# Optimization experiments

Hardware: AMD Instinct MI355X
Metric: run time of the kernel (lower is better)

## Reference

```python
import jax, jax.numpy as jnp
import numpy as np

N_NODES = 50000
N_EDGES = 800000
MUL0, MUL1 = 16, 8            # multiplicities of 0e and 1o irreps (input == output)
DIM_F = MUL0 + 3 * MUL1       # 40
NRB, NRD = 16, 64             # num_radial_basis, num_radial_dimension
MAX_RADIUS = 5.0
W_NUMEL = MUL0*MUL0 + MUL0*MUL1 + MUL1*MUL1 + MUL1*MUL0  # 576


def _radial_embedding(r):
    # e3nn soft_one_hot_linspace(basis='smooth_finite', cutoff=True), then *sqrt(NRB)
    values = jnp.linspace(0.0, MAX_RADIUS, NRB + 2)[1:-1]
    step = MAX_RADIUS / (NRB + 1)
    d = (r[:, None] - values) / step            # [E, NRB]
    inside = jnp.abs(d) < 1.0
    ds = jnp.where(inside, d, 0.0)              # safe values for the division
    y = 1.14136 * jnp.exp(jnp.float32(2.0)) * jnp.exp(-1.0 / (1.0 + ds)) * jnp.exp(-1.0 / (1.0 - ds))
    return jnp.where(inside, y, 0.0) * jnp.sqrt(jnp.float32(NRB))


def _forward(pos, f_in, W1, W2, edge_src, edge_dst):
    E = edge_src.shape[0]
    N = pos.shape[0]
    # edge geometry
    vec = pos[edge_dst] - pos[edge_src]                       # [E,3]
    r = jnp.sqrt(jnp.sum(vec * vec, axis=1) + 1e-12)          # [E]
    unit = vec / r[:, None]
    sh1 = jnp.sqrt(jnp.float32(3.0)) * unit                   # l=1 SH, component norm; sh0 == 1
    # radial MLP -> per-edge tensor-product weights (e3nn FullyConnectedNet scaling)
    emb = _radial_embedding(r)                                # [E, NRB]
    h = jax.nn.silu(emb @ W1 / jnp.sqrt(jnp.float32(NRB)))    # [E, NRD]
    w = h @ W2 / jnp.sqrt(jnp.float32(NRD))                   # [E, W_NUMEL]
    # gather source node features
    x = f_in[edge_src]                                        # [E, DIM_F]
    x0 = x[:, :MUL0]                                          # [E, 16] scalars (0e)
    x1 = x[:, MUL0:].reshape(E, MUL1, 3)                      # [E, 8, 3] vectors (1o)
    # split per-path 'uvw' weights
    o = MUL0 * MUL0
    w_00 = w[:, :o].reshape(E, MUL0, MUL0)                    # 0e x 0e -> 0e
    w_01 = w[:, o:o + MUL0*MUL1].reshape(E, MUL0, MUL1); o += MUL0*MUL1  # 0e x 1o -> 1o
    w_10 = w[:, o:o + MUL1*MUL1].reshape(E, MUL1, MUL1); o += MUL1*MUL1  # 1o x 0e -> 1o
    w_11 = w[:, o:o + MUL1*MUL0].reshape(E, MUL1, MUL0)                  # 1o x 1o -> 0e
    # path normalization: alpha = sqrt((2*l_out+1)/fan_in); fan_in per output = MUL0 + MUL1
    inv_fan = 1.0 / jnp.sqrt(jnp.float32(MUL0 + MUL1))
    inv_s3 = 1.0 / jnp.sqrt(jnp.float32(3.0))
    # scalar (0e) outputs
    dot = jnp.einsum('euk,ek->eu', x1, sh1)                   # [E, MUL1]
    out0 = inv_fan * (jnp.einsum('euw,eu->ew', w_00, x0)
                      + inv_s3 * jnp.einsum('euw,eu->ew', w_11, dot))
    # vector (1o) outputs
    out1 = inv_fan * (jnp.einsum('euw,eu->ew', w_01, x0)[:, :, None] * sh1[:, None, :]
                      + jnp.einsum('euw,euk->ewk', w_10, x1))
    summand = jnp.concatenate([out0, out1.reshape(E, 3 * MUL1)], axis=1)  # [E, DIM_F]
    f_out = jax.ops.segment_sum(summand, edge_dst, num_segments=N)
    num_neighbors = E / N
    return f_out / jnp.sqrt(jnp.float32(num_neighbors))


def setup_inputs() -> dict:
    key = jax.random.key(0)
    k1, k2, k3, k4, k5, k6 = jax.random.split(key, 6)
    pos = jax.random.normal(k1, (N_NODES, 3), dtype=jnp.float32)
    f_in = jax.random.normal(k2, (N_NODES, DIM_F), dtype=jnp.float32)
    edge_src = jax.random.randint(k3, (N_EDGES,), 0, N_NODES, dtype=jnp.int32)
    edge_dst = jax.random.randint(k4, (N_EDGES,), 0, N_NODES, dtype=jnp.int32)
    W1 = jax.random.normal(k5, (NRB, NRD), dtype=jnp.float32)
    W2 = jax.random.normal(k6, (NRD, W_NUMEL), dtype=jnp.float32)
    return {"pos": pos, "f_in": f_in, "edge_src": edge_src, "edge_dst": edge_dst, "W1": W1, "W2": W2}


def reference(pos, f_in, edge_src, edge_dst, W1, W2):
    return _forward(pos, f_in, W1, W2, edge_src, edge_dst)
```

## Files before the change

### kernel.cpp

```cpp
#include <hip/hip_runtime.h>
#include <hip/hip_fp16.h>

#define N_NODES 50000
#define N_EDGES 800000

typedef short  bf16x8 __attribute__((ext_vector_type(8)));
typedef float  f32x4  __attribute__((ext_vector_type(4)));
typedef _Float16 h16x2 __attribute__((ext_vector_type(2)));

#define FXP32_SCALE 4194304.0f
#define FXP32_INV   2.384185791015625e-07f

#define WSB_BYTES   (36864 * 2)

__device__ __forceinline__ unsigned short f2bf(float f) {
    unsigned u = __float_as_uint(f);
    u += 0x7FFF + ((u >> 16) & 1);
    return (unsigned short)(u >> 16);
}

__device__ __forceinline__ f32x4 fma4(f32x4 a, f32x4 b, f32x4 c) {
    f32x4 r;
    r[0] = fmaf(a[0], b[0], c[0]);
    r[1] = fmaf(a[1], b[1], c[1]);
    r[2] = fmaf(a[2], b[2], c[2]);
    r[3] = fmaf(a[3], b[3], c[3]);
    return r;
}

#if __has_builtin(__builtin_amdgcn_fdot2)
__device__ __forceinline__ float FDOT2(h16x2 a, h16x2 b, float c) {
    return __builtin_amdgcn_fdot2(a, b, c, false);
}
#else
__device__ __forceinline__ float FDOT2(h16x2 a, h16x2 b, float c) {
    return fmaf((float)a.x, (float)b.x, fmaf((float)a.y, (float)b.y, c));
}
#endif

__global__ void setup_kernel(const float* __restrict__ W2,
                             const float* __restrict__ W1,
                             unsigned short* __restrict__ wsB,
                             unsigned* __restrict__ w1p,
                             int4* __restrict__ out, int n16) {
    int gid = blockIdx.x * 256 + threadIdx.x;
    for (int i = gid; i < n16; i += gridDim.x * 256)
        out[i] = make_int4(0, 0, 0, 0);
    if (gid < 36864) {
        int j    = gid & 7;
        int lane = (gid >> 3) & 63;
        int ks   = (gid >> 9) & 1;
        int nt   = gid >> 10;
        int k = ks * 32 + (lane >> 4) * 8 + j;
        int n = nt * 16 + (lane & 15);
        wsB[gid] = f2bf(W2[k * 576 + n]);
    } else if (gid < 36864 + 512) {
        int idx = gid - 36864;
        int kk  = idx >> 6;
        int i   = idx & 63;
        __half lo = __float2half(W1[(2*kk)     * 64 + i]);
        __half hi = __float2half(W1[(2*kk + 1) * 64 + i]);
        w1p[idx] = (unsigned)__half_as_ushort(lo)
                 | ((unsigned)__half_as_ushort(hi) << 16);
    }
}

__global__ void finalize_kernel(float4* p, int n4) {
    int i = blockIdx.x * blockDim.x + threadIdx.x;
    if (i < n4) {
        float4 v = p[i];
        float4 f;
        f.x = (float)__float_as_int(v.x) * FXP32_INV;
        f.y = (float)__float_as_int(v.y) * FXP32_INV;
        f.z = (float)__float_as_int(v.z) * FXP32_INV;
        f.w = (float)__float_as_int(v.w) * FXP32_INV;
        p[i] = f;
    }
}

__global__ __launch_bounds__(64, 2) void conv_kernel(
    const float* __restrict__ pos,
    const float* __restrict__ f_in,
    const int*   __restrict__ esrc,
    const int*   __restrict__ edst,
    const unsigned* __restrict__ w1p,
    const unsigned short* __restrict__ wsB,
    int*         __restrict__ f_out_i)
{
    __shared__ __align__(16) char smem[9216];

    const int lane = threadIdx.x;
    const int e    = blockIdx.x * 64 + lane;
    char*  my  = smem;
    float* shf = (float*)smem;

    const int s = esrc[e];
    const int d = edst[e];

    const bf16x8* wsBv = (const bf16x8*)wsB;
    bf16x8 bc0 = wsBv[lane],        bc1 = wsBv[64 + lane];
    bf16x8 bn0 = wsBv[128 + lane],  bn1 = wsBv[192 + lane];
    bf16x8 b20, b21;

    float px = pos[3*d+0] - pos[3*s+0];
    float py = pos[3*d+1] - pos[3*s+1];
    float pz = pos[3*d+2] - pos[3*s+2];
    float r  = sqrtf(px*px + py*py + pz*pz + 1e-12f);
    float inv_r = __builtin_amdgcn_rcpf(r);
    float ux = px*inv_r, uy = py*inv_r, uz = pz*inv_r;
    const float SQ3 = 1.7320508075688772f;
    float shx = SQ3*ux, shy = SQ3*uy, shz = SQ3*uz;

    float x0[16], x1[24], dot[8];
    {
        const float4* xg4 = reinterpret_cast<const float4*>(f_in + (size_t)s * 40);
        float xr[40];
        #pragma unroll
        for (int q8 = 0; q8 < 10; ++q8) {
            float4 v = xg4[q8];
            xr[4*q8+0] = v.x; xr[4*q8+1] = v.y; xr[4*q8+2] = v.z; xr[4*q8+3] = v.w;
        }
        #pragma unroll
        for (int i = 0; i < 16; ++i) x0[i] = xr[i];
        #pragma unroll
        for (int i = 0; i < 24; ++i) x1[i] = xr[16+i];
        #pragma unroll
        for (int u = 0; u < 8; ++u)
            dot[u] = x1[3*u+0]*ux + x1[3*u+1]*uy + x1[3*u+2]*uz;
    }

    const float A = 1.14136f * 7.38905609893065f;
    const float inv_step = 17.0f / 5.0f;
    float emb[16];
    #pragma unroll
    for (int k = 0; k < 16; ++k) {
        float dd  = r * inv_step - (float)(k + 1);
        float d2v = dd * dd;
        float arg = -2.0f * __builtin_amdgcn_rcpf(1.0f - d2v);
        float val = A * __expf(arg);
        emb[k] = (d2v < 1.0f) ? val : 0.0f;
    }

    unsigned ep[8];
    #pragma unroll
    for (int kk = 0; kk < 8; ++kk) {
        __half lo = __float2half(emb[2*kk]);
        __half hi = __float2half(emb[2*kk+1]);
        ep[kk] = (unsigned)__half_as_ushort(lo)
               | ((unsigned)__half_as_ushort(hi) << 16);
    }
    float h[64];
    #pragma unroll
    for (int i = 0; i < 64; ++i) h[i] = 0.f;
    #pragma unroll
    for (int kk = 0; kk < 8; ++kk) {
        h16x2 ev = __builtin_bit_cast(h16x2, ep[kk]);
        const unsigned* wrow = w1p + kk * 64;
        #pragma unroll
        for (int i = 0; i < 64; ++i) {
            h16x2 wv = __builtin_bit_cast(h16x2, wrow[i]);
            h[i] = FDOT2(ev, wv, h[i]);
        }
    }
    #pragma unroll
    for (int i = 0; i < 64; ++i) {
        float z = h[i];
        h[i] = z * __builtin_amdgcn_rcpf(1.0f + __expf(-z));
    }

    {
        unsigned int hp[32];
        #pragma unroll
        for (int i = 0; i < 32; ++i)
            hp[i] = (unsigned)f2bf(h[2*i]) | ((unsigned)f2bf(h[2*i+1]) << 16);
        uint4* hrow = (uint4*)(my + lane * 144);
        #pragma unroll
        for (int g = 0; g < 8; ++g)
            hrow[g] = make_uint4(hp[4*g], hp[4*g+1], hp[4*g+2], hp[4*g+3]);
    }
    asm volatile("s_waitcnt lgkmcnt(0)" ::: "memory");

    const int q   = lane >> 4;
    const int col = lane & 15;
    const int q4  = q * 4;
    const int ucol = col >> 3;
    bf16x8 aF[4][2];
    #pragma unroll
    for (int mt = 0; mt < 4; ++mt)
        #pragma unroll
        for (int ks = 0; ks < 2; ++ks)
            aF[mt][ks] = *(const bf16x8*)(my + (mt*16 + col)*144 + q*16 + ks*64);
    asm volatile("s_waitcnt lgkmcnt(0)" ::: "memory");

    #pragma unroll
    for (int u = 0; u < 16; ++u) shf[u*64 + lane] = x0[u];
    #pragma unroll
    for (int u = 0; u < 8;  ++u) shf[1024 + u*64 + lane] = dot[u];
    asm volatile("s_waitcnt lgkmcnt(0)" ::: "memory");

    f32x4 out0d[4], t01d[4], o1bd[4][3];
    #pragma unroll
    for (int m = 0; m < 4; ++m) {
        out0d[m] = (f32x4){0.f,0.f,0.f,0.f};
        t01d[m]  = (f32x4){0.f,0.f,0.f,0.f};
        #pragma unroll
        for (int k = 0; k < 3; ++k) o1bd[m][k] = (f32x4){0.f,0.f,0.f,0.f};
    }

#define MFMA8() \
    f32x4 wr0 = {0.f,0.f,0.f,0.f}, wr1 = {0.f,0.f,0.f,0.f}; \
    f32x4 wr2 = {0.f,0.f,0.f,0.f}, wr3 = {0.f,0.f,0.f,0.f}; \
    wr0 = __builtin_amdgcn_mfma_f32_16x16x32_bf16(aF[0][0], bc0, wr0, 0,0,0); \
    wr1 = __builtin_amdgcn_mfma_f32_16x16x32_bf16(aF[1][0], bc0, wr1, 0,0,0); \
    wr2 = __builtin_amdgcn_mfma_f32_16x16x32_bf16(aF[2][0], bc0, wr2, 0,0,0); \
    wr3 = __builtin_amdgcn_mfma_f32_16x16x32_bf16(aF[3][0], bc0, wr3, 0,0,0); \
    wr0 = __builtin_amdgcn_mfma_f32_16x16x32_bf16(aF[0][1], bc1, wr0, 0,0,0); \
    wr1 = __builtin_amdgcn_mfma_f32_16x16x32_bf16(aF[1][1], bc1, wr1, 0,0,0); \
    wr2 = __builtin_amdgcn_mfma_f32_16x16x32_bf16(aF[2][1], bc1, wr2, 0,0,0); \
    wr3 = __builtin_amdgcn_mfma_f32_16x16x32_bf16(aF[3][1], bc1, wr3, 0,0,0);

#define PRE(NT2) { b20 = wsBv[(NT2)*128 + lane]; b21 = wsBv[(NT2)*128 + 64 + lane]; }
#define ROT()    { bc0 = bn0; bc1 = bn1; bn0 = b20; bn1 = b21; }

#define CONS4(ACC, BASEW) { \
    const float* xb_ = shf + (BASEW) + q4; \
    ACC[0] = fma4(wr0, *(const f32x4*)(xb_ +  0), ACC[0]); \
    ACC[1] = fma4(wr1, *(const f32x4*)(xb_ + 16), ACC[1]); \
    ACC[2] = fma4(wr2, *(const f32x4*)(xb_ + 32), ACC[2]); \
    ACC[3] = fma4(wr3, *(const f32x4*)(xb_ + 48), ACC[3]); }

    #pragma unroll
    for (int u = 0; u < 16; ++u) {
        PRE(u + 2);
        MFMA8();
        CONS4(out0d, u * 64);
        ROT();
    }
    #pragma unroll
    for (int t = 0; t < 8; ++t) {
        PRE(t < 6 ? 18 + t : 28 + (t - 6));
        MFMA8();
        CONS4(t01d, (2*t + ucol) * 64);
        ROT();
    }
    #pragma unroll
    for (int m = 0; m < 4; ++m)
        #pragma unroll
        for (int rr = 0; rr < 4; ++rr)
            t01d[m][rr] += __shfl_xor(t01d[m][rr], 8);

    #pragma unroll
    for (int u = 0; u < 8; ++u) {
        PRE(u < 6 ? 30 + u : 24 + (u - 6));
        MFMA8();
        CONS4(out0d, 1024 + u * 64);
        ROT();
    }

    asm volatile("s_waitcnt lgkmcnt(0)" ::: "memory");
    #pragma unroll
    for (int u = 0; u < 8; ++u)
        #pragma unroll
        for (int k = 0; k < 3; ++k)
            shf[(u*3 + k)*64 + lane] = x1[3*u + k];
    asm volatile("s_waitcnt lgkmcnt(0)" ::: "memory");

    #pragma unroll
    for (int t = 0; t < 4; ++t) {
        if (t < 2) PRE(26 + t);
        MFMA8();
        const int ub = (2*t + ucol) * 192 + q4;
#define W10_MT(MT, WR) { \
        f32x4 xv0 = *(const f32x4*)(shf + ub +   0 + 16*(MT)); \
        f32x4 xv1 = *(const f32x4*)(shf + ub +  64 + 16*(MT)); \
        f32x4 xv2 = *(const f32x4*)(shf + ub + 128 + 16*(MT)); \
        o1bd[MT][0] = fma4(WR, xv0, o1bd[MT][0]); \
        o1bd[MT][1] = fma4(WR, xv1, o1bd[MT][1]); \
        o1bd[MT][2] = fma4(WR, xv2, o1bd[MT][2]); }
        W10_MT(0, wr0) W10_MT(1, wr1) W10_MT(2, wr2) W10_MT(3, wr3)
#undef W10_MT
        ROT();
    }
#undef CONS4
#undef PRE
#undef ROT
#undef MFMA8
    #pragma unroll
    for (int m = 0; m < 4; ++m)
        #pragma unroll
        for (int k = 0; k < 3; ++k)
            #pragma unroll
            for (int rr = 0; rr < 4; ++rr)
                o1bd[m][k][rr] += __shfl_xor(o1bd[m][k][rr], 8);

    const float FXP_S = (1.0f / (32.0f * 4.898979485566356f)) * FXP32_SCALE;

    asm volatile("s_waitcnt lgkmcnt(0)" ::: "memory");
    #pragma unroll
    for (int m = 0; m < 4; ++m)
        #pragma unroll
        for (int rr = 0; rr < 4; ++rr)
            shf[(16*m + 4*q + rr) * 20 + col] = out0d[m][rr];
    shf[lane*20 + 16] = shx;
    shf[lane*20 + 17] = shy;
    shf[lane*20 + 18] = shz;
    ((int*)shf)[lane*20 + 19] = d;
    asm volatile("s_waitcnt lgkmcnt(0)" ::: "memory");

    #pragma unroll 4
    for (int it = 0; it < 16; ++it) {
        int p  = it * 64 + lane;
        int ee = p >> 4;
        int c  = p & 15;
        float v = shf[ee*20 + c];
        int dd  = ((int*)shf)[ee*20 + 19];
        atomicAdd(f_out_i + (size_t)dd*40 + c, __float2int_rn(v * FXP_S));
    }

    float shr[4][4][3];
    #pragma unroll
    for (int m = 0; m < 4; ++m)
        #pragma unroll
        for (int rr = 0; rr < 4; ++rr) {
            int eb = (16*m + 4*q + rr) * 20 + 16;
            shr[m][rr][0] = shf[eb + 0];
            shr[m][rr][1] = shf[eb + 1];
            shr[m][rr][2] = shf[eb + 2];
        }
    asm volatile("s_waitcnt lgkmcnt(0)" ::: "memory");
    if (col < 8) {
        #pragma unroll
        for (int m = 0; m < 4; ++m)
            #pragma unroll
            for (int rr = 0; rr < 4; ++rr)
                #pragma unroll
                for (int k = 0; k < 3; ++k) {
                    float fv = fmaf(t01d[m][rr], shr[m][rr][k], o1bd[m][k][rr]);
                    shf[(16*m + 4*q + rr) * 28 + 3*col + k] = fv;
                }
    }
    ((int*)shf)[lane*28 + 27] = d;
    asm volatile("s_waitcnt lgkmcnt(0)" ::: "memory");

    #pragma unroll 4
    for (int it = 0; it < 24; ++it) {
        int p  = it * 64 + lane;
        int ee = (p * 10923) >> 18;
        int c  = p - ee * 24;
        float v = shf[ee*28 + c];
        int dd  = ((int*)shf)[ee*28 + 27];
        atomicAdd(f_out_i + (size_t)dd*40 + 16 + c, __float2int_rn(v * FXP_S));
    }
}

extern "C" void kernel_launch(void* const* d_in, const int* in_sizes, int n_in,
                              void* d_out, int out_size, void* d_ws, size_t ws_size,
                              hipStream_t stream) {
    const float* pos  = (const float*)d_in[0];
    const float* f_in = (const float*)d_in[1];
    const int*   esrc = (const int*)  d_in[2];
    const int*   edst = (const int*)  d_in[3];
    const float* W1   = (const float*)d_in[4];
    const float* W2   = (const float*)d_in[5];
    float* out = (float*)d_out;

    unsigned short* wsB = (unsigned short*)d_ws;
    unsigned*       w1p = (unsigned*)((char*)d_ws + WSB_BYTES);

    const int nOut = N_NODES * 40;
    const int n16  = nOut / 4;

    setup_kernel<<<256, 256, 0, stream>>>(W2, W1, wsB, w1p, (int4*)out, n16);

    conv_kernel<<<N_EDGES / 64, 64, 0, stream>>>(
        pos, f_in, esrc, edst, w1p, wsB, (int*)out);

    finalize_kernel<<<(n16 + 255) / 256, 256, 0, stream>>>((float4*)out, n16);
}
```

Baseline: 260.4 us.

## Compute first radial MLP layer with bf16 MFMA instead of per-lane fdot2

Replaces the per-thread fp16 dot2 loop for the 16x64 first radial layer with 16x16x32 bf16 MFMA instructions. Embeddings are packed to bf16 and staged in shared memory (zero-padded to K=32), and W1 is pre-swizzled into MFMA A-fragment layout in setup. SiLU is then applied to the MFMA outputs, which are written straight into the existing shared-memory h rows. This cuts scalar VALU work and register pressure from the 64-wide h array, at the cost of half the MFMA K dimension being padding, extra LDS traffic, and lower precision (bf16 instead of fp16).

```diff
diff --git a/kernel.cpp b/kernel.cpp
--- a/kernel.cpp
+++ b/kernel.cpp
@@ -1,22 +1,26 @@
 #include <hip/hip_runtime.h>
-#include <hip/hip_fp16.h>
 
 #define N_NODES 50000
 #define N_EDGES 800000
 
 typedef short  bf16x8 __attribute__((ext_vector_type(8)));
 typedef float  f32x4  __attribute__((ext_vector_type(4)));
-typedef _Float16 h16x2 __attribute__((ext_vector_type(2)));
 
 #define FXP32_SCALE 4194304.0f
 #define FXP32_INV   2.384185791015625e-07f
 
 #define WSB_BYTES   (36864 * 2)
+#define W1T_ENTRIES 2048
+#define EOFF        4608
 
 __device__ __forceinline__ unsigned short f2bf(float f) {
     unsigned u = __float_as_uint(f);
     u += 0x7FFF + ((u >> 16) & 1);
     return (unsigned short)(u >> 16);
+}
+
+__device__ __forceinline__ unsigned pack2bf(float a, float b) {
+    return (unsigned)f2bf(a) | ((unsigned)f2bf(b) << 16);
 }
 
 __device__ __forceinline__ f32x4 fma4(f32x4 a, f32x4 b, f32x4 c) {
@@ -28,20 +32,10 @@
     return r;
 }
 
-#if __has_builtin(__builtin_amdgcn_fdot2)
-__device__ __forceinline__ float FDOT2(h16x2 a, h16x2 b, float c) {
-    return __builtin_amdgcn_fdot2(a, b, c, false);
-}
-#else
-__device__ __forceinline__ float FDOT2(h16x2 a, h16x2 b, float c) {
-    return fmaf((float)a.x, (float)b.x, fmaf((float)a.y, (float)b.y, c));
-}
-#endif
-
 __global__ void setup_kernel(const float* __restrict__ W2,
                              const float* __restrict__ W1,
                              unsigned short* __restrict__ wsB,
-                             unsigned* __restrict__ w1p,
+                             unsigned short* __restrict__ w1tf,
                              int4* __restrict__ out, int n16) {
     int gid = blockIdx.x * 256 + threadIdx.x;
     for (int i = gid; i < n16; i += gridDim.x * 256)
@@ -54,14 +48,14 @@
         int k = ks * 32 + (lane >> 4) * 8 + j;
         int n = nt * 16 + (lane & 15);
         wsB[gid] = f2bf(W2[k * 576 + n]);
-    } else if (gid < 36864 + 512) {
-        int idx = gid - 36864;
-        int kk  = idx >> 6;
-        int i   = idx & 63;
-        __half lo = __float2half(W1[(2*kk)     * 64 + i]);
-        __half hi = __float2half(W1[(2*kk + 1) * 64 + i]);
-        w1p[idx] = (unsigned)__half_as_ushort(lo)
-                 | ((unsigned)__half_as_ushort(hi) << 16);
+    } else if (gid < 36864 + W1T_ENTRIES) {
+        int idx  = gid - 36864;
+        int j    = idx & 7;
+        int lane = (idx >> 3) & 63;
+        int mt   = idx >> 9;
+        int k = (lane >> 4) * 8 + j;
+        int n = mt * 16 + (lane & 15);
+        w1tf[idx] = (k < 16) ? f2bf(W1[k * 64 + n]) : (unsigned short)0;
     }
 }
 
@@ -83,7 +77,7 @@
     const float* __restrict__ f_in,
     const int*   __restrict__ esrc,
     const int*   __restrict__ edst,
-    const unsigned* __restrict__ w1p,
+    const unsigned short* __restrict__ w1tf,
     const unsigned short* __restrict__ wsB,
     int*         __restrict__ f_out_i)
 {
@@ -97,10 +91,17 @@
     const int s = esrc[e];
     const int d = edst[e];
 
+    const int q   = lane >> 4;
+    const int col = lane & 15;
+
     const bf16x8* wsBv = (const bf16x8*)wsB;
     bf16x8 bc0 = wsBv[lane],        bc1 = wsBv[64 + lane];
     bf16x8 bn0 = wsBv[128 + lane],  bn1 = wsBv[192 + lane];
     bf16x8 b20, b21;
+    const bf16x8* w1tv = (const bf16x8*)w1tf;
+    bf16x8 aW[4];
+    #pragma unroll
+    for (int mt = 0; mt < 4; ++mt) aW[mt] = w1tv[mt * 64 + lane];
 
     float px = pos[3*d+0] - pos[3*s+0];
     float py = pos[3*d+1] - pos[3*s+1];
@@ -141,47 +142,47 @@
         emb[k] = (d2v < 1.0f) ? val : 0.0f;
     }
 
-    unsigned ep[8];
-    #pragma unroll
-    for (int kk = 0; kk < 8; ++kk) {
-        __half lo = __float2half(emb[2*kk]);
-        __half hi = __float2half(emb[2*kk+1]);
-        ep[kk] = (unsigned)__half_as_ushort(lo)
-               | ((unsigned)__half_as_ushort(hi) << 16);
-    }
-    float h[64];
-    #pragma unroll
-    for (int i = 0; i < 64; ++i) h[i] = 0.f;
-    #pragma unroll
-    for (int kk = 0; kk < 8; ++kk) {
-        h16x2 ev = __builtin_bit_cast(h16x2, ep[kk]);
-        const unsigned* wrow = w1p + kk * 64;
-        #pragma unroll
-        for (int i = 0; i < 64; ++i) {
-            h16x2 wv = __builtin_bit_cast(h16x2, wrow[i]);
-            h[i] = FDOT2(ev, wv, h[i]);
+    {
+        unsigned ep[8];
+        #pragma unroll
+        for (int kk = 0; kk < 8; ++kk) ep[kk] = pack2bf(emb[2*kk], emb[2*kk+1]);
+        uint4* erow = (uint4*)(my + EOFF + lane * 64);
+        erow[0] = make_uint4(ep[0], ep[1], ep[2], ep[3]);
+        erow[1] = make_uint4(ep[4], ep[5], ep[6], ep[7]);
+        erow[2] = make_uint4(0u, 0u, 0u, 0u);
+        erow[3] = make_uint4(0u, 0u, 0u, 0u);
+    }
+    asm volatile("s_waitcnt lgkmcnt(0)" ::: "memory");
+
+    bf16x8 bE[4];
+    #pragma unroll
+    for (int nt = 0; nt < 4; ++nt)
+        bE[nt] = *(const bf16x8*)(my + EOFF + (nt*16 + col)*64 + q*16);
+    asm volatile("s_waitcnt lgkmcnt(0)" ::: "memory");
+
+    #pragma unroll
+    for (int nt = 0; nt < 4; ++nt) {
+        f32x4 cH[4];
+        #pragma unroll
+        for (int mt = 0; mt < 4; ++mt) {
+            f32x4 z = {0.f, 0.f, 0.f, 0.f};
+            cH[mt] = __builtin_amdgcn_mfma_f32_16x16x32_bf16(aW[mt], bE[nt], z, 0, 0, 0);
         }
-    }
-    #pragma unroll
-    for (int i = 0; i < 64; ++i) {
-        float z = h[i];
-        h[i] = z * __builtin_amdgcn_rcpf(1.0f + __expf(-z));
-    }
-
-    {
-        unsigned int hp[32];
-        #pragma unroll
-        for (int i = 0; i < 32; ++i)
-            hp[i] = (unsigned)f2bf(h[2*i]) | ((unsigned)f2bf(h[2*i+1]) << 16);
-        uint4* hrow = (uint4*)(my + lane * 144);
-        #pragma unroll
-        for (int g = 0; g < 8; ++g)
-            hrow[g] = make_uint4(hp[4*g], hp[4*g+1], hp[4*g+2], hp[4*g+3]);
-    }
-    asm volatile("s_waitcnt lgkmcnt(0)" ::: "memory");
-
-    const int q   = lane >> 4;
-    const int col = lane & 15;
+        char* rowb = my + (nt*16 + col) * 144 + q * 8;
+        #pragma unroll
+        for (int mt = 0; mt < 4; ++mt) {
+            #pragma unroll
+            for (int rr = 0; rr < 4; ++rr) {
+                float z = cH[mt][rr];
+                cH[mt][rr] = z * __builtin_amdgcn_rcpf(1.0f + __expf(-z));
+            }
+            unsigned lo = pack2bf(cH[mt][0], cH[mt][1]);
+            unsigned hi = pack2bf(cH[mt][2], cH[mt][3]);
+            *(uint2*)(rowb + mt * 32) = make_uint2(lo, hi);
+        }
+    }
+    asm volatile("s_waitcnt lgkmcnt(0)" ::: "memory");
+
     const int q4  = q * 4;
     const int ucol = col >> 3;
     bf16x8 aF[4][2];
@@ -364,16 +365,16 @@
     const float* W2   = (const float*)d_in[5];
     float* out = (float*)d_out;
 
-    unsigned short* wsB = (unsigned short*)d_ws;
-    unsigned*       w1p = (unsigned*)((char*)d_ws + WSB_BYTES);
+    unsigned short* wsB  = (unsigned short*)d_ws;
+    unsigned short* w1tf = (unsigned short*)((char*)d_ws + WSB_BYTES);
 
     const int nOut = N_NODES * 40;
     const int n16  = nOut / 4;
 
-    setup_kernel<<<256, 256, 0, stream>>>(W2, W1, wsB, w1p, (int4*)out, n16);
+    setup_kernel<<<256, 256, 0, stream>>>(W2, W1, wsB, w1tf, (int4*)out, n16);
 
     conv_kernel<<<N_EDGES / 64, 64, 0, stream>>>(
-        pos, f_in, esrc, edst, w1p, wsB, (int*)out);
+        pos, f_in, esrc, edst, w1tf, wsB, (int*)out);
 
     finalize_kernel<<<(n16 + 255) / 256, 256, 0, stream>>>((float4*)out, n16);
 }
```

Result: no change. 258.1 us (-0.9%).

## Pack two fixed-point outputs into one 64-bit atomic add

Applied to the files above, without the earlier changes.

Scatter-add now packs two adjacent int32 fixed-point channel values into a single 64-bit atomicAdd. This halves the number of global atomic operations per edge. The finalize kernel recovers the high word by subtracting the borrow caused by a negative low word. This relies on the low 32-bit sum never overflowing into the high half incorrectly. The carry correction only tracks the sign of the final low word, so low-word overflow during accumulation could corrupt the high channel.

```diff
diff --git a/kernel.cpp b/kernel.cpp
--- a/kernel.cpp
+++ b/kernel.cpp
@@ -37,6 +37,13 @@
     return fmaf((float)a.x, (float)b.x, fmaf((float)a.y, (float)b.y, c));
 }
 #endif
+
+__device__ __forceinline__ unsigned long long pack_pair(float v0, float v1, float sc) {
+    int i0 = __float2int_rn(v0 * sc);
+    int i1 = __float2int_rn(v1 * sc);
+    return (((unsigned long long)(unsigned)i1) << 32)
+         + (unsigned long long)(long long)i0;
+}
 
 __global__ void setup_kernel(const float* __restrict__ W2,
                              const float* __restrict__ W1,
@@ -65,16 +72,18 @@
     }
 }
 
-__global__ void finalize_kernel(float4* p, int n4) {
+__global__ void finalize_kernel(uint4* p, int n16) {
     int i = blockIdx.x * blockDim.x + threadIdx.x;
-    if (i < n4) {
-        float4 v = p[i];
-        float4 f;
-        f.x = (float)__float_as_int(v.x) * FXP32_INV;
-        f.y = (float)__float_as_int(v.y) * FXP32_INV;
-        f.z = (float)__float_as_int(v.z) * FXP32_INV;
-        f.w = (float)__float_as_int(v.w) * FXP32_INV;
-        p[i] = f;
+    if (i < n16) {
+        uint4 v = p[i];
+        int lo0 = (int)v.x, hi0 = (int)v.y + (int)(v.x >> 31);
+        int lo1 = (int)v.z, hi1 = (int)v.w + (int)(v.z >> 31);
+        uint4 o;
+        o.x = __float_as_uint((float)lo0 * FXP32_INV);
+        o.y = __float_as_uint((float)hi0 * FXP32_INV);
+        o.z = __float_as_uint((float)lo1 * FXP32_INV);
+        o.w = __float_as_uint((float)hi1 * FXP32_INV);
+        p[i] = o;
     }
 }
 
@@ -85,7 +94,7 @@
     const int*   __restrict__ edst,
     const unsigned* __restrict__ w1p,
     const unsigned short* __restrict__ wsB,
-    int*         __restrict__ f_out_i)
+    unsigned long long* __restrict__ f_out_u)
 {
     __shared__ __align__(16) char smem[9216];
 
@@ -308,13 +317,14 @@
     asm volatile("s_waitcnt lgkmcnt(0)" ::: "memory");
 
     #pragma unroll 4
-    for (int it = 0; it < 16; ++it) {
+    for (int it = 0; it < 8; ++it) {
         int p  = it * 64 + lane;
-        int ee = p >> 4;
-        int c  = p & 15;
-        float v = shf[ee*20 + c];
+        int ee = p >> 3;
+        int cp = p & 7;
+        float v0 = shf[ee*20 + 2*cp];
+        float v1 = shf[ee*20 + 2*cp + 1];
         int dd  = ((int*)shf)[ee*20 + 19];
-        atomicAdd(f_out_i + (size_t)dd*40 + c, __float2int_rn(v * FXP_S));
+        atomicAdd(f_out_u + (size_t)dd*20 + cp, pack_pair(v0, v1, FXP_S));
     }
 
     float shr[4][4][3];
@@ -343,13 +353,14 @@
     asm volatile("s_waitcnt lgkmcnt(0)" ::: "memory");
 
     #pragma unroll 4
-    for (int it = 0; it < 24; ++it) {
+    for (int it = 0; it < 12; ++it) {
         int p  = it * 64 + lane;
-        int ee = (p * 10923) >> 18;
-        int c  = p - ee * 24;
-        float v = shf[ee*28 + c];
+        int ee = (p * 21846) >> 18;
+        int jp = p - ee * 12;
+        float v0 = shf[ee*28 + 2*jp];
+        float v1 = shf[ee*28 + 2*jp + 1];
         int dd  = ((int*)shf)[ee*28 + 27];
-        atomicAdd(f_out_i + (size_t)dd*40 + 16 + c, __float2int_rn(v * FXP_S));
+        atomicAdd(f_out_u + (size_t)dd*20 + 8 + jp, pack_pair(v0, v1, FXP_S));
     }
 }
 
@@ -373,7 +384,7 @@
     setup_kernel<<<256, 256, 0, stream>>>(W2, W1, wsB, w1p, (int4*)out, n16);
 
     conv_kernel<<<N_EDGES / 64, 64, 0, stream>>>(
-        pos, f_in, esrc, edst, w1p, wsB, (int*)out);
-
-    finalize_kernel<<<(n16 + 255) / 256, 256, 0, stream>>>((float4*)out, n16);
-}
+        pos, f_in, esrc, edst, w1p, wsB, (unsigned long long*)out);
+
+    finalize_kernel<<<(n16 + 255) / 256, 256, 0, stream>>>((uint4*)out, n16);
+}
```

New measurement: 262.9 us. About the same (+1.0%).

## Fuse setup, convolution and finalize into one persistent cooperative kernel

Applied to the files above, without the earlier changes.

Replaces the three launches (zero/pack, edge convolution, fixed-point finalize) with a single cooperative persistent kernel. Grid-wide syncs separate the phases, and each block loops over edge tiles. The aim is to remove launch gaps and tail effects between kernels. In exchange it adds two grid barriers, caps the grid at occupancy × 256 (max 2048) blocks, and keeps the old three-kernel path as a fallback.

```diff
diff --git a/kernel.cpp b/kernel.cpp
--- a/kernel.cpp
+++ b/kernel.cpp
@@ -1,8 +1,12 @@
 #include <hip/hip_runtime.h>
 #include <hip/hip_fp16.h>
+#include <hip/hip_cooperative_groups.h>
+
+namespace cg = cooperative_groups;
 
 #define N_NODES 50000
 #define N_EDGES 800000
+#define N_TILES (N_EDGES / 64)
 
 typedef short  bf16x8 __attribute__((ext_vector_type(8)));
 typedef float  f32x4  __attribute__((ext_vector_type(4)));
@@ -38,24 +42,21 @@
 }
 #endif
 
-__global__ void setup_kernel(const float* __restrict__ W2,
-                             const float* __restrict__ W1,
-                             unsigned short* __restrict__ wsB,
-                             unsigned* __restrict__ w1p,
-                             int4* __restrict__ out, int n16) {
-    int gid = blockIdx.x * 256 + threadIdx.x;
-    for (int i = gid; i < n16; i += gridDim.x * 256)
-        out[i] = make_int4(0, 0, 0, 0);
-    if (gid < 36864) {
-        int j    = gid & 7;
-        int lane = (gid >> 3) & 63;
-        int ks   = (gid >> 9) & 1;
-        int nt   = gid >> 10;
+__device__ __forceinline__ void pack_item(int p,
+                                          const float* __restrict__ W2,
+                                          const float* __restrict__ W1,
+                                          unsigned short* __restrict__ wsB,
+                                          unsigned* __restrict__ w1p) {
+    if (p < 36864) {
+        int j    = p & 7;
+        int lane = (p >> 3) & 63;
+        int ks   = (p >> 9) & 1;
+        int nt   = p >> 10;
         int k = ks * 32 + (lane >> 4) * 8 + j;
         int n = nt * 16 + (lane & 15);
-        wsB[gid] = f2bf(W2[k * 576 + n]);
-    } else if (gid < 36864 + 512) {
-        int idx = gid - 36864;
+        wsB[p] = f2bf(W2[k * 576 + n]);
+    } else {
+        int idx = p - 36864;
         int kk  = idx >> 6;
         int i   = idx & 63;
         __half lo = __float2half(W1[(2*kk)     * 64 + i]);
@@ -65,34 +66,28 @@
     }
 }
 
-__global__ void finalize_kernel(float4* p, int n4) {
-    int i = blockIdx.x * blockDim.x + threadIdx.x;
-    if (i < n4) {
-        float4 v = p[i];
-        float4 f;
-        f.x = (float)__float_as_int(v.x) * FXP32_INV;
-        f.y = (float)__float_as_int(v.y) * FXP32_INV;
-        f.z = (float)__float_as_int(v.z) * FXP32_INV;
-        f.w = (float)__float_as_int(v.w) * FXP32_INV;
-        p[i] = f;
-    }
-}
-
-__global__ __launch_bounds__(64, 2) void conv_kernel(
+__device__ __forceinline__ float4 finalize4(float4 v) {
+    float4 f;
+    f.x = (float)__float_as_int(v.x) * FXP32_INV;
+    f.y = (float)__float_as_int(v.y) * FXP32_INV;
+    f.z = (float)__float_as_int(v.z) * FXP32_INV;
+    f.w = (float)__float_as_int(v.w) * FXP32_INV;
+    return f;
+}
+
+__device__ __forceinline__ void conv_tile(
+    int tile, int lane,
     const float* __restrict__ pos,
     const float* __restrict__ f_in,
     const int*   __restrict__ esrc,
     const int*   __restrict__ edst,
     const unsigned* __restrict__ w1p,
     const unsigned short* __restrict__ wsB,
-    int*         __restrict__ f_out_i)
+    int*         __restrict__ f_out_i,
+    char*        my)
 {
-    __shared__ __align__(16) char smem[9216];
-
-    const int lane = threadIdx.x;
-    const int e    = blockIdx.x * 64 + lane;
-    char*  my  = smem;
-    float* shf = (float*)smem;
+    float* shf = (float*)my;
+    const int e = tile * 64 + lane;
 
     const int s = esrc[e];
     const int d = edst[e];
@@ -351,6 +346,79 @@
         int dd  = ((int*)shf)[ee*28 + 27];
         atomicAdd(f_out_i + (size_t)dd*40 + 16 + c, __float2int_rn(v * FXP_S));
     }
+
+    asm volatile("s_waitcnt lgkmcnt(0)" ::: "memory");
+}
+
+__global__ __launch_bounds__(64, 2) void fused_kernel(
+    const float* __restrict__ pos,
+    const float* __restrict__ f_in,
+    const int*   __restrict__ esrc,
+    const int*   __restrict__ edst,
+    const float* __restrict__ W1,
+    const float* __restrict__ W2,
+    unsigned short* __restrict__ wsB,
+    unsigned* __restrict__ w1p,
+    int*      __restrict__ f_out_i)
+{
+    __shared__ __align__(16) char smem[9216];
+    const int lane = threadIdx.x;
+    const int gid  = blockIdx.x * 64 + lane;
+    const int nth  = gridDim.x * 64;
+
+    {
+        int4* outz = (int4*)f_out_i;
+        const int n16 = (N_NODES * 40) / 4;
+        for (int i = gid; i < n16; i += nth)
+            outz[i] = make_int4(0, 0, 0, 0);
+        for (int p = gid; p < 36864 + 512; p += nth)
+            pack_item(p, W2, W1, wsB, w1p);
+    }
+    __threadfence();
+    cg::this_grid().sync();
+
+    for (int tile = blockIdx.x; tile < N_TILES; tile += gridDim.x)
+        conv_tile(tile, lane, pos, f_in, esrc, edst, w1p, wsB, f_out_i, smem);
+
+    __threadfence();
+    cg::this_grid().sync();
+
+    {
+        float4* p4 = (float4*)f_out_i;
+        const int n16 = (N_NODES * 40) / 4;
+        for (int i = gid; i < n16; i += nth)
+            p4[i] = finalize4(p4[i]);
+    }
+}
+
+__global__ void setup_kernel(const float* __restrict__ W2,
+                             const float* __restrict__ W1,
+                             unsigned short* __restrict__ wsB,
+                             unsigned* __restrict__ w1p,
+                             int4* __restrict__ out, int n16) {
+    int gid = blockIdx.x * 256 + threadIdx.x;
+    for (int i = gid; i < n16; i += gridDim.x * 256)
+        out[i] = make_int4(0, 0, 0, 0);
+    if (gid < 36864 + 512) pack_item(gid, W2, W1, wsB, w1p);
+}
+
+__global__ void finalize_kernel(float4* p, int n4) {
+    int i = blockIdx.x * blockDim.x + threadIdx.x;
+    if (i < n4) p[i] = finalize4(p[i]);
+}
+
+__global__ __launch_bounds__(64, 2) void conv_kernel(
+    const float* __restrict__ pos,
+    const float* __restrict__ f_in,
+    const int*   __restrict__ esrc,
+    const int*   __restrict__ edst,
+    const unsigned* __restrict__ w1p,
+    const unsigned short* __restrict__ wsB,
+    int*         __restrict__ f_out_i)
+{
+    __shared__ __align__(16) char smem[9216];
+    conv_tile(blockIdx.x, threadIdx.x, pos, f_in, esrc, edst, w1p, wsB,
+              f_out_i, smem);
 }
 
 extern "C" void kernel_launch(void* const* d_in, const int* in_sizes, int n_in,
@@ -366,14 +434,39 @@
 
     unsigned short* wsB = (unsigned short*)d_ws;
     unsigned*       w1p = (unsigned*)((char*)d_ws + WSB_BYTES);
+    int*            outi = (int*)out;
 
     const int nOut = N_NODES * 40;
     const int n16  = nOut / 4;
 
+    static int coop_blocks = -2;
+    if (coop_blocks == -2) {
+        int dev = 0, coop = 0, nblk = 0;
+        if (hipGetDevice(&dev) == hipSuccess &&
+            hipDeviceGetAttribute(&coop, hipDeviceAttributeCooperativeLaunch,
+                                  dev) == hipSuccess && coop) {
+            if (hipOccupancyMaxActiveBlocksPerMultiprocessor(
+                    &nblk, (const void*)fused_kernel, 64, 0) == hipSuccess &&
+                nblk > 0) {
+                coop_blocks = nblk * 256;
+                if (coop_blocks > 2048) coop_blocks = 2048;
+            } else coop_blocks = -1;
+        } else coop_blocks = -1;
+    }
+
+    if (coop_blocks > 0) {
+        void* args[] = {(void*)&pos, (void*)&f_in, (void*)&esrc, (void*)&edst,
+                        (void*)&W1, (void*)&W2, (void*)&wsB, (void*)&w1p,
+                        (void*)&outi};
+        hipError_t err = hipLaunchCooperativeKernel(
+            (const void*)fused_kernel, dim3(coop_blocks), dim3(64),
+            args, 0, stream);
+        if (err == hipSuccess) return;
+        (void)hipGetLastError();
+        coop_blocks = -1;
+    }
+
     setup_kernel<<<256, 256, 0, stream>>>(W2, W1, wsB, w1p, (int4*)out, n16);
-
-    conv_kernel<<<N_EDGES / 64, 64, 0, stream>>>(
-        pos, f_in, esrc, edst, w1p, wsB, (int*)out);
-
+    conv_kernel<<<N_TILES, 64, 0, stream>>>(pos, f_in, esrc, edst, w1p, wsB, outi);
     finalize_kernel<<<(n16 + 255) / 256, 256, 0, stream>>>((float4*)out, n16);
 }
```

Result: slower. 943.8 us (+262.5%).
